# Kernel tuning notes

Measured on AMD Instinct MI355X. Metric: run time of the kernel, lower is better.

## Reference

```python
import jax, jax.numpy as jnp
import numpy as np

TAU = 0.25            # leaky-integrator time constant
OUTPUT_TICKS = 4      # inference output_ticks
T, B, P, H, S, C = 20, 16384, 256, 512, 512, 128  # timesteps, batch, pho, hidden_ps, sem, sem_cleanup


def setup_inputs() -> dict:
    key = jax.random.key(0)
    ks = jax.random.split(key, 9)
    u = lambda k, shape: jax.random.uniform(k, shape, jnp.float32, -0.1, 0.1)
    return {
        "inputs": jax.random.normal(ks[0], (T, B, P), jnp.float32),
        "w_hps_ph": u(ks[1], (P, H)),
        "w_hps_hs": u(ks[2], (H, S)),
        "w_ss": u(ks[3], (S, S)),
        "w_sc": u(ks[4], (S, C)),
        "w_cs": u(ks[5], (C, S)),
        "bias_hps": u(ks[6], (H,)),
        "bias_s": u(ks[7], (S,)),
        "bias_css": u(ks[8], (C,)),
    }


def reference(inputs, w_hps_ph, w_hps_hs, w_ss, w_sc, w_cs, bias_hps, bias_s, bias_css):
    """HS04 task_pho_sem, inference mode (no weight noise).
    Leaky-integrator recurrence over timesteps; returns sigmoid semantic
    activations for the last OUTPUT_TICKS steps: (OUTPUT_TICKS, B, S)."""
    n_t, b, _ = inputs.shape
    h = w_hps_ph.shape[1]
    s_dim = w_ss.shape[0]
    c_dim = w_cs.shape[0]
    sig = jax.nn.sigmoid
    one_m_tau = 1.0 - TAU

    init = (
        jnp.zeros((b, h), jnp.float32),   # input_hps
        jnp.zeros((b, s_dim), jnp.float32),  # input_s
        jnp.zeros((b, c_dim), jnp.float32),  # input_css
        jnp.full((b, h), 0.5, jnp.float32),  # act_hps
        jnp.full((b, s_dim), 0.5, jnp.float32),  # act_s
        jnp.full((b, c_dim), 0.5, jnp.float32),  # act_css
    )

    def step(carry, x_t):
        in_hps, in_s, in_css, a_hps, a_s, a_css = carry
        hps = TAU * (x_t @ w_hps_ph + bias_hps) + one_m_tau * in_hps
        s = TAU * (a_hps @ w_hps_hs + a_s @ w_ss + a_css @ w_cs + bias_s) + one_m_tau * in_s
        css = TAU * (a_s @ w_sc + bias_css) + one_m_tau * in_css
        a_s_new = sig(s)
        new_carry = (hps, s, css, sig(hps), a_s_new, sig(css))
        return new_carry, a_s_new

    _, act_s_all = jax.lax.scan(step, init, inputs)  # (T, B, S)
    return act_s_all[-OUTPUT_TICKS:]
```

## Files before the change

### kernel.cpp

```cpp
#include <hip/hip_runtime.h>

#define TAU 0.25f
#define OMT 0.75f

typedef __attribute__((ext_vector_type(8))) short  bfrag8;
typedef __attribute__((ext_vector_type(4))) float  f4acc;
typedef __attribute__((ext_vector_type(4))) float  fvec4;
typedef __attribute__((ext_vector_type(2))) unsigned uvec2;
typedef __attribute__((ext_vector_type(4))) unsigned uvec4;

#define WS_PACKH 0u
#define WS_PACKS 262144u
#define WS_PACKC 1441792u
#define WS_BIAS  1572864u

__device__ __forceinline__ unsigned short f2bf(float f) {
    unsigned u = __builtin_bit_cast(unsigned, f);
    u = (u + 0x7FFFu + ((u >> 16) & 1u)) >> 16;
    return (unsigned short)u;
}

__global__ void hs04_prep(const float* __restrict__ wph, const float* __restrict__ whs,
                          const float* __restrict__ wss, const float* __restrict__ wsc,
                          const float* __restrict__ wcs, const float* __restrict__ bh,
                          const float* __restrict__ bs,  const float* __restrict__ bc,
                          unsigned char* __restrict__ ws)
{
    int gid = blockIdx.x * 256 + threadIdx.x;
    if (gid < 98304) {
        int lane = gid & 63, frag = gid >> 6;
        int cls, nt, ks; size_t off;
        if (frag < 256)       { cls = 0; nt = frag >> 3;       ks = frag & 7;
                                off = WS_PACKH + (size_t)nt*8192  + (size_t)ks*1024; }
        else if (frag < 1408) { int f = frag - 256;  cls = 1; nt = f / 36; ks = f - nt*36;
                                off = WS_PACKS + (size_t)nt*36864 + (size_t)ks*1024; }
        else                  { int f = frag - 1408; cls = 2; nt = f >> 4; ks = f & 15;
                                off = WS_PACKC + (size_t)nt*16384 + (size_t)ks*1024; }
        int q = lane >> 4, rr = lane & 15;
        unsigned short v[8];
        #pragma unroll
        for (int j = 0; j < 8; ++j) {
            int k = ks*32 + q*8 + j;
            int n = nt*16 + rr;
            float wv;
            if (cls == 0)      wv = wph[k*512 + n];
            else if (cls == 1) wv = (k < 512)  ? whs[k*512 + n]
                               : (k < 1024) ? wss[(k-512)*512 + n]
                                            : wcs[(k-1024)*512 + n];
            else               wv = wsc[k*128 + n];
            v[j] = f2bf(wv);
        }
        uvec4 pk = { (unsigned)v[0] | ((unsigned)v[1] << 16),
                     (unsigned)v[2] | ((unsigned)v[3] << 16),
                     (unsigned)v[4] | ((unsigned)v[5] << 16),
                     (unsigned)v[6] | ((unsigned)v[7] << 16) };
        *(uvec4*)(ws + off + (size_t)lane*16) = pk;
    } else if (gid < 98304 + 1152) {
        int col = gid - 98304;
        float b = (col < 512) ? bh[col] : (col < 1024 ? bs[col-512] : bc[col-1024]);
        ((float*)(ws + WS_BIAS))[col] = TAU * b;
    }
}

__global__ __launch_bounds__(512, 2) void hs04_main(const float* __restrict__ x_all,
                                                    const unsigned char* __restrict__ ws,
                                                    float* __restrict__ out)
{
    extern __shared__ char smem[];
    char* const acts = smem;
    char* const xbuf = smem + 147456;

    const int tid  = threadIdx.x;
    const int lane = tid & 63;
    const int w    = tid >> 6;
    const int q    = lane >> 4;
    const int r    = lane & 15;
    const int b0   = blockIdx.x << 6;

    {
        unsigned hv = f2bf(0.125f);
        unsigned u  = hv | (hv << 16);
        uvec4 fill = {u, u, u, u};
        uvec4* p = (uvec4*)acts;
        for (int i = tid; i < 9216; i += 512) p[i] = fill;
    }

    int colbase[9];
    #pragma unroll
    for (int j = 0; j < 4; ++j) { colbase[j] = w*64 + j*16; colbase[4+j] = 512 + w*64 + j*16; }
    colbase[8] = 1024 + w*16;

    float tb[9];
    {
        const float* bias = (const float*)(ws + WS_BIAS);
        #pragma unroll
        for (int j = 0; j < 9; ++j) tb[j] = bias[colbase[j] + r];
    }

    f4acc acc[9][4];
    #pragma unroll
    for (int j = 0; j < 9; ++j)
        #pragma unroll
        for (int m = 0; m < 4; ++m) acc[j][m] = {0.f, 0.f, 0.f, 0.f};

    const bfrag8* bH[4]; const bfrag8* bS[4]; const bfrag8* bC;
    #pragma unroll
    for (int j = 0; j < 4; ++j) {
        bH[j] = (const bfrag8*)(ws + WS_PACKH + (size_t)(w*4+j)*8192)  + lane;
        bS[j] = (const bfrag8*)(ws + WS_PACKS + (size_t)(w*4+j)*36864) + lane;
    }
    bC = (const bfrag8*)(ws + WS_PACKC + (size_t)w*16384) + lane;

    __syncthreads();

    for (int t = 0; t < 20; ++t) {
        #pragma unroll
        for (int j = 0; j < 9; ++j) {
            float tbj = tb[j];
            #pragma unroll
            for (int m = 0; m < 4; ++m) {
                f4acc a = acc[j][m];
                a.x = OMT*a.x + tbj; a.y = OMT*a.y + tbj;
                a.z = OMT*a.z + tbj; a.w = OMT*a.w + tbj;
                acc[j][m] = a;
            }
        }

        const float* xt = x_all + ((size_t)t*16384 + (size_t)b0) * 256;
        auto stageX = [&](int mt, char* dst) {
            const fvec4* src = (const fvec4*)xt + (size_t)mt*1024;
            #pragma unroll
            for (int i = 0; i < 2; ++i) {
                int f4i = tid + i*512;
                fvec4 v = src[f4i];
                int row = f4i >> 6;
                int c4  = f4i & 63;
                unsigned lo = (unsigned)f2bf(TAU*v.x) | ((unsigned)f2bf(TAU*v.y) << 16);
                unsigned hi = (unsigned)f2bf(TAU*v.z) | ((unsigned)f2bf(TAU*v.w) << 16);
                int phys = (c4 >> 1) ^ row;
                uvec2 d = {lo, hi};
                *(uvec2*)(dst + row*512 + phys*16 + ((c4 & 1) << 3)) = d;
            }
        };
        stageX(0, xbuf);
        __syncthreads();
        #pragma unroll
        for (int mt = 0; mt < 4; ++mt) {
            if (mt < 3) stageX(mt+1, xbuf + ((mt+1)&1)*8192);
            const char* xb = xbuf + (mt&1)*8192;
            #pragma unroll 2
            for (int ks = 0; ks < 8; ++ks) {
                bfrag8 af = *(const bfrag8*)(xb + r*512 + ((((ks<<2)+q) ^ r) << 4));
                #pragma unroll
                for (int j = 0; j < 4; ++j) {
                    bfrag8 bf = bH[j][ks*64];
                    acc[j][mt] = __builtin_amdgcn_mfma_f32_16x16x32_bf16(af, bf, acc[j][mt], 0, 0, 0);
                }
            }
            __syncthreads();
        }

        #pragma unroll 2
        for (int ks = 0; ks < 36; ++ks) {
            bfrag8 a[4];
            #pragma unroll
            for (int m = 0; m < 4; ++m)
                a[m] = *(const bfrag8*)(acts + (m*16 + r)*2304 + ((((ks<<2)+q) ^ r) << 4));
            #pragma unroll
            for (int j = 0; j < 4; ++j) {
                bfrag8 bf = bS[j][ks*64];
                #pragma unroll
                for (int m = 0; m < 4; ++m)
                    acc[4+j][m] = __builtin_amdgcn_mfma_f32_16x16x32_bf16(a[m], bf, acc[4+j][m], 0, 0, 0);
            }
            if (ks >= 16 && ks < 32) {
                bfrag8 bf = bC[(ks-16)*64];
                #pragma unroll
                for (int m = 0; m < 4; ++m)
                    acc[8][m] = __builtin_amdgcn_mfma_f32_16x16x32_bf16(a[m], bf, acc[8][m], 0, 0, 0);
            }
        }

        __syncthreads();
        {
            const bool emit = (t >= 16);
            #pragma unroll
            for (int j = 0; j < 9; ++j) {
                int col   = colbase[j] + r;
                int chunk = col >> 3;
                int coff  = (col & 7) << 1;
                #pragma unroll
                for (int m = 0; m < 4; ++m) {
                    f4acc v = acc[j][m];
                    #pragma unroll
                    for (int e = 0; e < 4; ++e) {
                        int rl  = q*4 + e;
                        int row = m*16 + rl;
                        float in = (e==0)?v.x:(e==1)?v.y:(e==2)?v.z:v.w;
                        float a  = 1.0f / (1.0f + __expf(-in));
                        *(unsigned short*)(acts + row*2304 + ((chunk ^ rl) << 4) + coff) = f2bf(TAU * a);
                        if (emit && j >= 4 && j < 8) {
                            float* op = out + (((size_t)(t-16)*16384 + (size_t)(b0 + row)) * 512);
                            op[col - 512] = a;
                        }
                    }
                }
            }
        }
        __syncthreads();
    }
}

extern "C" void kernel_launch(void* const* d_in, const int* in_sizes, int n_in,
                              void* d_out, int out_size, void* d_ws, size_t ws_size,
                              hipStream_t stream) {
    const float* x   = (const float*)d_in[0];
    const float* wph = (const float*)d_in[1];
    const float* whs = (const float*)d_in[2];
    const float* wss = (const float*)d_in[3];
    const float* wsc = (const float*)d_in[4];
    const float* wcs = (const float*)d_in[5];
    const float* bh  = (const float*)d_in[6];
    const float* bs  = (const float*)d_in[7];
    const float* bc  = (const float*)d_in[8];
    unsigned char* ws = (unsigned char*)d_ws;
    float* outp = (float*)d_out;

    hipFuncSetAttribute((const void*)hs04_main,
                        hipFuncAttributeMaxDynamicSharedMemorySize, 163840);

    hipLaunchKernelGGL(hs04_prep, dim3(389), dim3(256), 0, stream,
                       wph, whs, wss, wsc, wcs, bh, bs, bc, ws);
    hipLaunchKernelGGL(hs04_main, dim3(256), dim3(512), 163840, stream,
                       x, ws, outp);
}
```

Baseline: 2.638 ms.

## Software-pipeline weight/activation fragment loads and prefetch next-step inputs across recurrence

Restructures the per-timestep loops so B-weight and A-activation fragments are double-buffered in registers, issuing the next k-slice's global and LDS loads before the current MFMAs. Input staging for the next timestep is now loaded during the tail of the semantic GEMM and written to LDS afterwards, which removes one barrier-separated staging phase per step. The leaky decay and bias are folded into the epilogue, nontemporal loads and stores are used for streamed x and output, and the wave index is made scalar via readfirstlane. The extra double-buffered fragments raise register pressure, which could cause spills under the 512x2 launch bounds.

```diff
diff --git a/kernel.cpp b/kernel.cpp
--- a/kernel.cpp
+++ b/kernel.cpp
@@ -72,7 +72,7 @@
 
     const int tid  = threadIdx.x;
     const int lane = tid & 63;
-    const int w    = tid >> 6;
+    const int wu   = __builtin_amdgcn_readfirstlane(tid >> 6);
     const int q    = lane >> 4;
     const int r    = lane & 15;
     const int b0   = blockIdx.x << 6;
@@ -85,100 +85,145 @@
         for (int i = tid; i < 9216; i += 512) p[i] = fill;
     }
 
-    int colbase[9];
-    #pragma unroll
-    for (int j = 0; j < 4; ++j) { colbase[j] = w*64 + j*16; colbase[4+j] = 512 + w*64 + j*16; }
-    colbase[8] = 1024 + w*16;
-
     float tb[9];
     {
         const float* bias = (const float*)(ws + WS_BIAS);
         #pragma unroll
-        for (int j = 0; j < 9; ++j) tb[j] = bias[colbase[j] + r];
+        for (int j = 0; j < 9; ++j) {
+            int cb = (j < 4) ? wu*64 + j*16 : (j < 8) ? 512 + wu*64 + (j-4)*16 : 1024 + wu*16;
+            tb[j] = bias[cb + r];
+        }
     }
 
     f4acc acc[9][4];
     #pragma unroll
-    for (int j = 0; j < 9; ++j)
-        #pragma unroll
-        for (int m = 0; m < 4; ++m) acc[j][m] = {0.f, 0.f, 0.f, 0.f};
-
-    const bfrag8* bH[4]; const bfrag8* bS[4]; const bfrag8* bC;
+    for (int j = 0; j < 9; ++j) {
+        float tbj = tb[j];
+        #pragma unroll
+        for (int m = 0; m < 4; ++m) acc[j][m] = {tbj, tbj, tbj, tbj};
+    }
+
+    const bfrag8* bHp[4]; const bfrag8* bSp[4]; const bfrag8* bCp;
     #pragma unroll
     for (int j = 0; j < 4; ++j) {
-        bH[j] = (const bfrag8*)(ws + WS_PACKH + (size_t)(w*4+j)*8192)  + lane;
-        bS[j] = (const bfrag8*)(ws + WS_PACKS + (size_t)(w*4+j)*36864) + lane;
-    }
-    bC = (const bfrag8*)(ws + WS_PACKC + (size_t)w*16384) + lane;
-
-    __syncthreads();
-
-    for (int t = 0; t < 20; ++t) {
-        #pragma unroll
-        for (int j = 0; j < 9; ++j) {
-            float tbj = tb[j];
-            #pragma unroll
-            for (int m = 0; m < 4; ++m) {
-                f4acc a = acc[j][m];
-                a.x = OMT*a.x + tbj; a.y = OMT*a.y + tbj;
-                a.z = OMT*a.z + tbj; a.w = OMT*a.w + tbj;
-                acc[j][m] = a;
-            }
-        }
-
-        const float* xt = x_all + ((size_t)t*16384 + (size_t)b0) * 256;
-        auto stageX = [&](int mt, char* dst) {
-            const fvec4* src = (const fvec4*)xt + (size_t)mt*1024;
-            #pragma unroll
-            for (int i = 0; i < 2; ++i) {
-                int f4i = tid + i*512;
-                fvec4 v = src[f4i];
-                int row = f4i >> 6;
-                int c4  = f4i & 63;
-                unsigned lo = (unsigned)f2bf(TAU*v.x) | ((unsigned)f2bf(TAU*v.y) << 16);
-                unsigned hi = (unsigned)f2bf(TAU*v.z) | ((unsigned)f2bf(TAU*v.w) << 16);
-                int phys = (c4 >> 1) ^ row;
-                uvec2 d = {lo, hi};
-                *(uvec2*)(dst + row*512 + phys*16 + ((c4 & 1) << 3)) = d;
-            }
-        };
-        stageX(0, xbuf);
-        __syncthreads();
-        #pragma unroll
-        for (int mt = 0; mt < 4; ++mt) {
-            if (mt < 3) stageX(mt+1, xbuf + ((mt+1)&1)*8192);
-            const char* xb = xbuf + (mt&1)*8192;
-            #pragma unroll 2
-            for (int ks = 0; ks < 8; ++ks) {
-                bfrag8 af = *(const bfrag8*)(xb + r*512 + ((((ks<<2)+q) ^ r) << 4));
-                #pragma unroll
-                for (int j = 0; j < 4; ++j) {
-                    bfrag8 bf = bH[j][ks*64];
-                    acc[j][mt] = __builtin_amdgcn_mfma_f32_16x16x32_bf16(af, bf, acc[j][mt], 0, 0, 0);
-                }
-            }
-            __syncthreads();
-        }
-
-        #pragma unroll 2
-        for (int ks = 0; ks < 36; ++ks) {
-            bfrag8 a[4];
+        bHp[j] = (const bfrag8*)(ws + WS_PACKH + (size_t)(wu*4+j)*8192)  + lane;
+        bSp[j] = (const bfrag8*)(ws + WS_PACKS + (size_t)(wu*4+j)*36864) + lane;
+    }
+    bCp = (const bfrag8*)(ws + WS_PACKC + (size_t)wu*16384) + lane;
+
+    auto stageX_load = [&](const float* xt, int mt, fvec4 (&v)[2]) {
+        const fvec4* src = (const fvec4*)xt + (size_t)mt*1024;
+        v[0] = __builtin_nontemporal_load(src + tid);
+        v[1] = __builtin_nontemporal_load(src + tid + 512);
+    };
+    auto stageX_write = [&](const fvec4 (&v)[2], char* dst) {
+        #pragma unroll
+        for (int i = 0; i < 2; ++i) {
+            int f4i = tid + i*512;
+            int row = f4i >> 6, c4 = f4i & 63;
+            unsigned lo = (unsigned)f2bf(TAU*v[i].x) | ((unsigned)f2bf(TAU*v[i].y) << 16);
+            unsigned hi = (unsigned)f2bf(TAU*v[i].z) | ((unsigned)f2bf(TAU*v[i].w) << 16);
+            uvec2 d = {lo, hi};
+            *(uvec2*)(dst + row*512 + (((c4 >> 1) ^ row) << 4) + ((c4 & 1) << 3)) = d;
+        }
+    };
+    auto loadBS = [&](int ks, bfrag8 (&d)[4]) {
+        #pragma unroll
+        for (int j = 0; j < 4; ++j) d[j] = bSp[j][ks*64];
+    };
+    auto loadA2 = [&](int ks, bfrag8 (&d)[4]) {
+        const char* p = acts + r*2304 + ((((ks << 2) + q) ^ r) << 4);
+        #pragma unroll
+        for (int m = 0; m < 4; ++m) d[m] = *(const bfrag8*)(p + m*36864);
+    };
+    auto mm16 = [&](bfrag8 (&a)[4], bfrag8 (&b)[4]) {
+        #pragma unroll
+        for (int j = 0; j < 4; ++j)
             #pragma unroll
             for (int m = 0; m < 4; ++m)
-                a[m] = *(const bfrag8*)(acts + (m*16 + r)*2304 + ((((ks<<2)+q) ^ r) << 4));
+                acc[4+j][m] = __builtin_amdgcn_mfma_f32_16x16x32_bf16(a[m], b[j], acc[4+j][m], 0, 0, 0);
+    };
+    auto mmc = [&](bfrag8 (&a)[4], bfrag8 c) {
+        #pragma unroll
+        for (int m = 0; m < 4; ++m)
+            acc[8][m] = __builtin_amdgcn_mfma_f32_16x16x32_bf16(a[m], c, acc[8][m], 0, 0, 0);
+    };
+
+    {
+        fvec4 xv0[2];
+        stageX_load(x_all + (size_t)b0*256, 0, xv0);
+        stageX_write(xv0, xbuf);
+    }
+    __syncthreads();
+
+    for (int t = 0; t < 20; ++t) {
+        const float* xt = x_all + ((size_t)t*16384 + (size_t)b0)*256;
+        fvec4 xv[2];
+
+        #pragma unroll
+        for (int mt = 0; mt < 4; ++mt) {
+            if (mt < 3) stageX_load(xt, mt+1, xv);
+            const char* xb = xbuf + (mt & 1)*8192;
+            bfrag8 hb0[4], hb1[4];
             #pragma unroll
-            for (int j = 0; j < 4; ++j) {
-                bfrag8 bf = bS[j][ks*64];
+            for (int j = 0; j < 4; ++j) hb0[j] = bHp[j][0];
+            #pragma unroll 1
+            for (int k2 = 0; k2 < 8; k2 += 2) {
                 #pragma unroll
-                for (int m = 0; m < 4; ++m)
-                    acc[4+j][m] = __builtin_amdgcn_mfma_f32_16x16x32_bf16(a[m], bf, acc[4+j][m], 0, 0, 0);
-            }
-            if (ks >= 16 && ks < 32) {
-                bfrag8 bf = bC[(ks-16)*64];
-                #pragma unroll
-                for (int m = 0; m < 4; ++m)
-                    acc[8][m] = __builtin_amdgcn_mfma_f32_16x16x32_bf16(a[m], bf, acc[8][m], 0, 0, 0);
-            }
+                for (int j = 0; j < 4; ++j) hb1[j] = bHp[j][(k2+1)*64];
+                {
+                    bfrag8 ha = *(const bfrag8*)(xb + r*512 + ((((k2 << 2) + q) ^ r) << 4));
+                    #pragma unroll
+                    for (int j = 0; j < 4; ++j)
+                        acc[j][mt] = __builtin_amdgcn_mfma_f32_16x16x32_bf16(ha, hb0[j], acc[j][mt], 0, 0, 0);
+                }
+                if (k2 + 2 < 8) {
+                    #pragma unroll
+                    for (int j = 0; j < 4; ++j) hb0[j] = bHp[j][(k2+2)*64];
+                }
+                {
+                    bfrag8 ha = *(const bfrag8*)(xb + r*512 + (((((k2+1) << 2) + q) ^ r) << 4));
+                    #pragma unroll
+                    for (int j = 0; j < 4; ++j)
+                        acc[j][mt] = __builtin_amdgcn_mfma_f32_16x16x32_bf16(ha, hb1[j], acc[j][mt], 0, 0, 0);
+                }
+            }
+            if (mt < 3) {
+                stageX_write(xv, xbuf + ((mt+1) & 1)*8192);
+                __syncthreads();
+            }
+        }
+
+        {
+            bfrag8 sa0[4], sa1[4], sb0[4], sb1[4];
+            loadBS(0, sb0); loadA2(0, sa0);
+            #pragma unroll 1
+            for (int ks = 0; ks < 16; ks += 2) {
+                loadBS(ks+1, sb1); loadA2(ks+1, sa1);
+                mm16(sa0, sb0);
+                loadBS(ks+2, sb0); loadA2(ks+2, sa0);
+                mm16(sa1, sb1);
+            }
+            #pragma unroll 1
+            for (int ks = 16; ks < 32; ks += 2) {
+                bfrag8 c0 = bCp[(ks-16)*64];
+                loadBS(ks+1, sb1); loadA2(ks+1, sa1);
+                mm16(sa0, sb0);
+                mmc(sa0, c0);
+                bfrag8 c1 = bCp[(ks-15)*64];
+                loadBS(ks+2, sb0); loadA2(ks+2, sa0);
+                mm16(sa1, sb1);
+                mmc(sa1, c1);
+            }
+            if (t < 19) stageX_load(xt + 16384*256, 0, xv);
+            #pragma unroll 1
+            for (int ks = 32; ks < 36; ks += 2) {
+                loadBS(ks+1, sb1); loadA2(ks+1, sa1);
+                mm16(sa0, sb0);
+                if (ks + 2 < 36) { loadBS(ks+2, sb0); loadA2(ks+2, sa0); }
+                mm16(sa1, sb1);
+            }
+            if (t < 19) stageX_write(xv, xbuf);
         }
 
         __syncthreads();
@@ -186,9 +231,11 @@
             const bool emit = (t >= 16);
             #pragma unroll
             for (int j = 0; j < 9; ++j) {
-                int col   = colbase[j] + r;
+                int cb = (j < 4) ? wu*64 + j*16 : (j < 8) ? 512 + wu*64 + (j-4)*16 : 1024 + wu*16;
+                int col   = cb + r;
                 int chunk = col >> 3;
                 int coff  = (col & 7) << 1;
+                float tbj = tb[j];
                 #pragma unroll
                 for (int m = 0; m < 4; ++m) {
                     f4acc v = acc[j][m];
@@ -196,14 +243,15 @@
                     for (int e = 0; e < 4; ++e) {
                         int rl  = q*4 + e;
                         int row = m*16 + rl;
-                        float in = (e==0)?v.x:(e==1)?v.y:(e==2)?v.z:v.w;
+                        float in = v[e];
                         float a  = 1.0f / (1.0f + __expf(-in));
                         *(unsigned short*)(acts + row*2304 + ((chunk ^ rl) << 4) + coff) = f2bf(TAU * a);
                         if (emit && j >= 4 && j < 8) {
-                            float* op = out + (((size_t)(t-16)*16384 + (size_t)(b0 + row)) * 512);
-                            op[col - 512] = a;
+                            __builtin_nontemporal_store(
+                                a, out + ((size_t)(t-16)*16384 + (size_t)(b0 + row))*512 + (col - 512));
                         }
                     }
+                    acc[j][m] = v*OMT + tbj;
                 }
             }
         }
```

Measured after the change: 2.118 ms. -19.7%, faster.
